# Kernel optimization log

Measured on AMD Instinct MI355X. Metric: run time of the kernel, lower is better.

## Reference

```python
import jax, jax.numpy as jnp
import numpy as np

B, N, D = 16, 2048, 64


def setup_inputs() -> dict:
    key = jax.random.key(0)
    kq, kk, kv = jax.random.split(key, 3)
    queries = jax.random.normal(kq, (B, N, D), dtype=jnp.float32)
    keys = jax.random.normal(kk, (B, N, D), dtype=jnp.float32)
    values = jax.random.normal(kv, (B, N, D), dtype=jnp.float32)
    return {"queries": queries, "keys": keys, "values": values}


def reference(queries, keys, values):
    d = queries.shape[-1]
    scale = 1.0 / jnp.sqrt(jnp.asarray(d, dtype=queries.dtype))
    # scores: [B, N, N] = Q @ K^T / sqrt(d)
    scores = jnp.einsum("bqd,bkd->bqk", queries, keys) * scale
    attn = jax.nn.softmax(scores, axis=-1)
    # dropout prob = 0.0 -> identity (inference-faithful)
    out = jnp.einsum("bqk,bkd->bqd", attn, values)
    return out
```

## Files before the change

kernel.cpp:

```cpp
#include <hip/hip_runtime.h>

typedef __attribute__((ext_vector_type(8)))  __bf16 bf16x8;
typedef __attribute__((ext_vector_type(4)))  __bf16 bf16x4;
typedef __attribute__((ext_vector_type(16))) float  f32x16;
typedef __attribute__((ext_vector_type(4)))  float  f32x4;

#define B_    16
#define N_    2048
#define D_    64
#define QBLK  128
#define KVBLK 64
#define NT    (N_ / KVBLK)
#define NG    4
#define TPG   (NT / NG)

#define VSTR    80
#define KSZ     8192
#define VASZ    5120
#define SLOT_SZ (KSZ + 2 * VASZ)
#define GRP_SZ  (2 * SLOT_SZ)
#define SMEM_SZ (NG * GRP_SZ)

static __device__ __forceinline__ float fast_exp2(float x) {
#if __has_builtin(__builtin_amdgcn_exp2f)
    return __builtin_amdgcn_exp2f(x);
#else
    return __expf(x * 0.6931471805599453f);
#endif
}

__global__ __attribute__((amdgpu_waves_per_eu(4, 4))) __launch_bounds__(1024)
void attn_fwd(const float* __restrict__ Qp, const float* __restrict__ Kp,
              const float* __restrict__ Vp, float* __restrict__ Op)
{
    __shared__ __align__(16) char smem[SMEM_SZ];

    const int tid  = threadIdx.x;
    const int wv   = tid >> 6;
    const int g    = tid >> 8;
    const int tg   = tid & 255;
    const int lane = tid & 63;
    const int w    = (tid >> 6) & 3;
    const int h    = lane >> 5;
    const int qcol = lane & 31;
    const int first  = (wv ^ (wv >> 2)) & 1;
    const int second = first ^ 1;

    const int bx    = blockIdx.x;
    const int batch = ((bx & 7) << 1) | ((bx >> 3) & 1);
    const int qtile = bx >> 4;
    const int q0w   = qtile * QBLK + w * 32;

    const float SL2E = 0.18033688011112042f;
    const size_t bboff = (size_t)batch * (N_ * D_);
    char* gbase = smem + g * GRP_SZ;

    const float* qrow = Qp + bboff + (size_t)(q0w + qcol) * D_ + h * 8;
    bf16x8 qf[4];
#pragma unroll
    for (int m = 0; m < 4; ++m) {
        f32x4 a = *reinterpret_cast<const f32x4*>(qrow + m * 16);
        f32x4 b = *reinterpret_cast<const f32x4*>(qrow + m * 16 + 4);
#pragma unroll
        for (int j = 0; j < 4; ++j) {
            qf[m][j]     = (__bf16)(a[j] * SL2E);
            qf[m][4 + j] = (__bf16)(b[j] * SL2E);
        }
    }

    const int krow = tg >> 3,  kcol = (tg & 7) * 8;
    const int vd   = tg & 63,  vkg  = tg >> 6;
    const int p1   = (vkg & 1) * 8 + (vkg >> 1) * 32;
    const int xorv = ((vd >> 3) & 3) << 4;
    const float* ksrc0 = Kp + bboff + (size_t)krow * D_ + kcol;
    const float* vsrc0 = Vp + bboff + (size_t)(vkg * 8) * D_ + vd;

    f32x4 kr[2];
    float vv[8];
    auto load_phase = [&](int t, int ph) {
        const float* ks = ksrc0 + ((size_t)t * KVBLK + ph * 32) * D_;
        const float* vs = vsrc0 + ((size_t)t * KVBLK + ph * 32) * D_;
        kr[0] = *reinterpret_cast<const f32x4*>(ks);
        kr[1] = *reinterpret_cast<const f32x4*>(ks + 4);
#pragma unroll
        for (int j = 0; j < 8; ++j) vv[j] = vs[(size_t)j * D_];
    };

    auto write_phase = [&](int b, int ph) {
        char* kb = gbase + b * SLOT_SZ;
        char* vb = kb + KSZ + ph * VASZ;
        bf16x8 w0;
#pragma unroll
        for (int j = 0; j < 4; ++j) { w0[j] = (__bf16)kr[0][j]; w0[4 + j] = (__bf16)kr[1][j]; }
        *reinterpret_cast<bf16x8*>(kb + (ph * 32 + krow) * 128 +
                                   ((kcol * 2) ^ ((krow & 7) << 4))) = w0;
        bf16x4 w1, w2;
#pragma unroll
        for (int j = 0; j < 4; ++j) { w1[j] = (__bf16)vv[j]; w2[j] = (__bf16)vv[4 + j]; }
        char* vrow = vb + vd * VSTR;
        *reinterpret_cast<bf16x4*>(vrow + ((p1)      ^ xorv)) = w1;
        *reinterpret_cast<bf16x4*>(vrow + ((p1 + 16) ^ xorv)) = w2;
    };

    f32x16 o0, o1;
#pragma unroll
    for (int i = 0; i < 16; ++i) { o0[i] = 0.f; o1[i] = 0.f; }
    float l_run = 0.f;

    const int kx  = (qcol & 7) << 4;
    const int vxr = ((qcol >> 3) & 3) << 4;

    auto do_sub = [&](const char* kb, int sub, int nxt, bool more) {
        f32x16 s;
#pragma unroll
        for (int i = 0; i < 16; ++i) s[i] = 0.f;
        __builtin_amdgcn_s_setprio(1);
#pragma unroll
        for (int m = 0; m < 4; ++m) {
            const int col = m * 32 + h * 16;
            bf16x8 k0 = *reinterpret_cast<const bf16x8*>(
                kb + (sub * 32 + qcol) * 128 + (col ^ kx));
            s = __builtin_amdgcn_mfma_f32_32x32x16_bf16(k0, qf[m], s, 0, 0, 0);
        }
        __builtin_amdgcn_s_setprio(0);

        float ps0 = 0.f, ps1 = 0.f, ps2 = 0.f, ps3 = 0.f;
        bf16x8 pfa, pfb;
#pragma unroll
        for (int i = 0; i < 4; ++i) {
            float p0 = fast_exp2(s[i]);
            float p1e = fast_exp2(s[4 + i]);
            float p2 = fast_exp2(s[8 + i]);
            float p3 = fast_exp2(s[12 + i]);
            ps0 += p0; ps1 += p1e; ps2 += p2; ps3 += p3;
            pfa[i] = (__bf16)p0; pfa[4 + i] = (__bf16)p1e;
            pfb[i] = (__bf16)p2; pfb[4 + i] = (__bf16)p3;
        }
        l_run += (ps0 + ps1) + (ps2 + ps3);

        if (more) write_phase(nxt, sub);

        const char* vb = kb + KSZ + sub * VASZ;
        __builtin_amdgcn_s_setprio(1);
#pragma unroll
        for (int db = 0; db < 2; ++db) {
            const char* vrowp = vb + (db * 32 + qcol) * VSTR;
            f32x16& oo = db ? o1 : o0;
#pragma unroll
            for (int sc = 0; sc < 2; ++sc) {
                bf16x8 vf = *reinterpret_cast<const bf16x8*>(
                    vrowp + ((h * 16 + sc * 32) ^ vxr));
                oo = __builtin_amdgcn_mfma_f32_32x32x16_bf16(vf, sc ? pfb : pfa, oo, 0, 0, 0);
            }
        }
        __builtin_amdgcn_s_setprio(0);
    };

    load_phase(g, 0);  write_phase(0, 0);
    load_phase(g, 1);  write_phase(0, 1);
    __syncthreads();

    for (int it = 0; it < TPG; ++it) {
        const int cur = it & 1;
        const int nxt = cur ^ 1;
        const bool more = (it + 1 < TPG);
        const int tn = NG * (it + 1) + g;
        const char* kb = gbase + cur * SLOT_SZ;

        if (more) load_phase(tn, first);
        do_sub(kb, first, nxt, more);
        if (more) load_phase(tn, second);
        do_sub(kb, second, nxt, more);
        __syncthreads();
    }

    float lt = l_run + __shfl_xor(l_run, 32);
    float* mlF  = (float*)smem;
    float* slab = (float*)smem;
    const int q  = w * 32 + qcol;

    if (h == 0) mlF[g * QBLK + q] = lt;
    __syncthreads();

    const float L = mlF[0 * QBLK + q] + mlF[1 * QBLK + q]
                  + mlF[2 * QBLK + q] + mlF[3 * QBLK + q];
    const float inv = 1.0f / L;
    __syncthreads();

    const int dl0 = 4 * h;
    auto slab_write = [&](float* sb, const f32x16& oo, int db) {
#pragma unroll
        for (int r = 0; r < 16; ++r) {
            const int d = db * 32 + (r & 3) + 8 * (r >> 2) + dl0;
            sb[d * 128 + q] = oo[r];
        }
    };
    auto slab_add = [&](const float* sb, f32x16& oo, int db) {
#pragma unroll
        for (int r = 0; r < 16; ++r) {
            const int d = db * 32 + (r & 3) + 8 * (r >> 2) + dl0;
            oo[r] += sb[d * 128 + q];
        }
    };

    if (g == 1) { slab_write(slab, o0, 0);        slab_write(slab, o1, 1); }
    if (g == 3) { slab_write(slab + 8192, o0, 0); slab_write(slab + 8192, o1, 1); }
    __syncthreads();

    if (g == 0) { slab_add(slab, o0, 0);        slab_add(slab, o1, 1); }
    if (g == 2) { slab_add(slab + 8192, o0, 0); slab_add(slab + 8192, o1, 1); }
    __syncthreads();

    if (g == 2) { slab_write(slab, o0, 0); slab_write(slab, o1, 1); }
    __syncthreads();

    if (g == 0) {
#pragma unroll
        for (int r = 0; r < 16; ++r) {
            const int d0 = (r & 3) + 8 * (r >> 2) + dl0;
            o0[r] = (o0[r] + slab[d0 * 128 + q]) * inv;
            o1[r] = (o1[r] + slab[(32 + d0) * 128 + q]) * inv;
        }
        float* orow = Op + bboff + (size_t)(q0w + qcol) * D_;
#pragma unroll
        for (int gg8 = 0; gg8 < 4; ++gg8) {
            f32x4 v, v2;
#pragma unroll
            for (int r = 0; r < 4; ++r) { v[r] = o0[4 * gg8 + r]; v2[r] = o1[4 * gg8 + r]; }
            *reinterpret_cast<f32x4*>(orow + gg8 * 8 + 4 * h)      = v;
            *reinterpret_cast<f32x4*>(orow + 32 + gg8 * 8 + 4 * h) = v2;
        }
    }
}

extern "C" void kernel_launch(void* const* d_in, const int* in_sizes, int n_in,
                              void* d_out, int out_size, void* d_ws, size_t ws_size,
                              hipStream_t stream) {
    const float* Q = (const float*)d_in[0];
    const float* K = (const float*)d_in[1];
    const float* V = (const float*)d_in[2];
    float* O = (float*)d_out;
    dim3 grid(256), block(1024);
    hipLaunchKernelGGL(attn_fwd, grid, block, 0, stream, Q, K, V, O);
}
```

Before: 34.02 us.

## Halve query and KV tiles, use 512-thread blocks with a single-subtile loop

```diff
diff --git a/kernel.cpp b/kernel.cpp
--- a/kernel.cpp
+++ b/kernel.cpp
@@ -8,16 +8,15 @@
 #define B_    16
 #define N_    2048
 #define D_    64
-#define QBLK  128
-#define KVBLK 64
+#define QBLK  64
+#define KVBLK 32
 #define NT    (N_ / KVBLK)
 #define NG    4
 #define TPG   (NT / NG)
 
 #define VSTR    80
-#define KSZ     8192
-#define VASZ    5120
-#define SLOT_SZ (KSZ + 2 * VASZ)
+#define KSZ     4096
+#define SLOT_SZ 9216
 #define GRP_SZ  (2 * SLOT_SZ)
 #define SMEM_SZ (NG * GRP_SZ)
 
@@ -29,7 +28,7 @@
 #endif
 }
 
-__global__ __attribute__((amdgpu_waves_per_eu(4, 4))) __launch_bounds__(1024)
+__global__ __attribute__((amdgpu_waves_per_eu(4, 4))) __launch_bounds__(512)
 void attn_fwd(const float* __restrict__ Qp, const float* __restrict__ Kp,
               const float* __restrict__ Vp, float* __restrict__ Op)
 {
@@ -37,14 +36,12 @@
 
     const int tid  = threadIdx.x;
     const int wv   = tid >> 6;
-    const int g    = tid >> 8;
-    const int tg   = tid & 255;
+    const int g    = wv >> 1;
+    const int w    = wv & 1;
+    const int tg   = tid & 127;
     const int lane = tid & 63;
-    const int w    = (tid >> 6) & 3;
     const int h    = lane >> 5;
     const int qcol = lane & 31;
-    const int first  = (wv ^ (wv >> 2)) & 1;
-    const int second = first ^ 1;
 
     const int bx    = blockIdx.x;
     const int batch = ((bx & 7) << 1) | ((bx >> 3) & 1);
@@ -69,17 +66,17 @@
     }
 
     const int krow = tg >> 3,  kcol = (tg & 7) * 8;
-    const int vd   = tg & 63,  vkg  = tg >> 6;
-    const int p1   = (vkg & 1) * 8 + (vkg >> 1) * 32;
+    const int vd   = tg & 63,  vkl  = tg >> 6;
+    const int p1l  = vkl * 8;
     const int xorv = ((vd >> 3) & 3) << 4;
     const float* ksrc0 = Kp + bboff + (size_t)krow * D_ + kcol;
-    const float* vsrc0 = Vp + bboff + (size_t)(vkg * 8) * D_ + vd;
+    const float* vsrc0 = Vp + bboff + (size_t)(vkl * 8) * D_ + vd;
 
     f32x4 kr[2];
     float vv[8];
     auto load_phase = [&](int t, int ph) {
-        const float* ks = ksrc0 + ((size_t)t * KVBLK + ph * 32) * D_;
-        const float* vs = vsrc0 + ((size_t)t * KVBLK + ph * 32) * D_;
+        const float* ks = ksrc0 + ((size_t)t * KVBLK + ph * 16) * D_;
+        const float* vs = vsrc0 + ((size_t)t * KVBLK + ph * 16) * D_;
         kr[0] = *reinterpret_cast<const f32x4*>(ks);
         kr[1] = *reinterpret_cast<const f32x4*>(ks + 4);
 #pragma unroll
@@ -88,16 +85,17 @@
 
     auto write_phase = [&](int b, int ph) {
         char* kb = gbase + b * SLOT_SZ;
-        char* vb = kb + KSZ + ph * VASZ;
+        char* vb = kb + KSZ;
         bf16x8 w0;
 #pragma unroll
         for (int j = 0; j < 4; ++j) { w0[j] = (__bf16)kr[0][j]; w0[4 + j] = (__bf16)kr[1][j]; }
-        *reinterpret_cast<bf16x8*>(kb + (ph * 32 + krow) * 128 +
+        *reinterpret_cast<bf16x8*>(kb + (ph * 16 + krow) * 128 +
                                    ((kcol * 2) ^ ((krow & 7) << 4))) = w0;
         bf16x4 w1, w2;
 #pragma unroll
         for (int j = 0; j < 4; ++j) { w1[j] = (__bf16)vv[j]; w2[j] = (__bf16)vv[4 + j]; }
         char* vrow = vb + vd * VSTR;
+        const int p1 = p1l + ph * 32;
         *reinterpret_cast<bf16x4*>(vrow + ((p1)      ^ xorv)) = w1;
         *reinterpret_cast<bf16x4*>(vrow + ((p1 + 16) ^ xorv)) = w2;
     };
@@ -110,7 +108,19 @@
     const int kx  = (qcol & 7) << 4;
     const int vxr = ((qcol >> 3) & 3) << 4;
 
-    auto do_sub = [&](const char* kb, int sub, int nxt, bool more) {
+    load_phase(g, 0);  write_phase(0, 0);
+    load_phase(g, 1);  write_phase(0, 1);
+    __syncthreads();
+
+    for (int it = 0; it < TPG; ++it) {
+        const int cur = it & 1;
+        const int nxt = cur ^ 1;
+        const bool more = (it + 1 < TPG);
+        const int tn = NG * (it + 1) + g;
+        const char* kb = gbase + cur * SLOT_SZ;
+
+        if (more) load_phase(tn, 0);
+
         f32x16 s;
 #pragma unroll
         for (int i = 0; i < 16; ++i) s[i] = 0.f;
@@ -118,8 +128,7 @@
 #pragma unroll
         for (int m = 0; m < 4; ++m) {
             const int col = m * 32 + h * 16;
-            bf16x8 k0 = *reinterpret_cast<const bf16x8*>(
-                kb + (sub * 32 + qcol) * 128 + (col ^ kx));
+            bf16x8 k0 = *reinterpret_cast<const bf16x8*>(kb + qcol * 128 + (col ^ kx));
             s = __builtin_amdgcn_mfma_f32_32x32x16_bf16(k0, qf[m], s, 0, 0, 0);
         }
         __builtin_amdgcn_s_setprio(0);
@@ -138,9 +147,9 @@
         }
         l_run += (ps0 + ps1) + (ps2 + ps3);
 
-        if (more) write_phase(nxt, sub);
-
-        const char* vb = kb + KSZ + sub * VASZ;
+        if (more) { write_phase(nxt, 0); load_phase(tn, 1); }
+
+        const char* vb = kb + KSZ;
         __builtin_amdgcn_s_setprio(1);
 #pragma unroll
         for (int db = 0; db < 2; ++db) {
@@ -154,23 +163,8 @@
             }
         }
         __builtin_amdgcn_s_setprio(0);
-    };
-
-    load_phase(g, 0);  write_phase(0, 0);
-    load_phase(g, 1);  write_phase(0, 1);
-    __syncthreads();
-
-    for (int it = 0; it < TPG; ++it) {
-        const int cur = it & 1;
-        const int nxt = cur ^ 1;
-        const bool more = (it + 1 < TPG);
-        const int tn = NG * (it + 1) + g;
-        const char* kb = gbase + cur * SLOT_SZ;
-
-        if (more) load_phase(tn, first);
-        do_sub(kb, first, nxt, more);
-        if (more) load_phase(tn, second);
-        do_sub(kb, second, nxt, more);
+
+        if (more) write_phase(nxt, 1);
         __syncthreads();
     }
 
@@ -192,23 +186,23 @@
 #pragma unroll
         for (int r = 0; r < 16; ++r) {
             const int d = db * 32 + (r & 3) + 8 * (r >> 2) + dl0;
-            sb[d * 128 + q] = oo[r];
+            sb[d * QBLK + q] = oo[r];
         }
     };
     auto slab_add = [&](const float* sb, f32x16& oo, int db) {
 #pragma unroll
         for (int r = 0; r < 16; ++r) {
             const int d = db * 32 + (r & 3) + 8 * (r >> 2) + dl0;
-            oo[r] += sb[d * 128 + q];
+            oo[r] += sb[d * QBLK + q];
         }
     };
 
     if (g == 1) { slab_write(slab, o0, 0);        slab_write(slab, o1, 1); }
-    if (g == 3) { slab_write(slab + 8192, o0, 0); slab_write(slab + 8192, o1, 1); }
+    if (g == 3) { slab_write(slab + 4096, o0, 0); slab_write(slab + 4096, o1, 1); }
     __syncthreads();
 
     if (g == 0) { slab_add(slab, o0, 0);        slab_add(slab, o1, 1); }
-    if (g == 2) { slab_add(slab + 8192, o0, 0); slab_add(slab + 8192, o1, 1); }
+    if (g == 2) { slab_add(slab + 4096, o0, 0); slab_add(slab + 4096, o1, 1); }
     __syncthreads();
 
     if (g == 2) { slab_write(slab, o0, 0); slab_write(slab, o1, 1); }
@@ -218,8 +212,8 @@
 #pragma unroll
         for (int r = 0; r < 16; ++r) {
             const int d0 = (r & 3) + 8 * (r >> 2) + dl0;
-            o0[r] = (o0[r] + slab[d0 * 128 + q]) * inv;
-            o1[r] = (o1[r] + slab[(32 + d0) * 128 + q]) * inv;
+            o0[r] = (o0[r] + slab[d0 * QBLK + q]) * inv;
+            o1[r] = (o1[r] + slab[(32 + d0) * QBLK + q]) * inv;
         }
         float* orow = Op + bboff + (size_t)(q0w + qcol) * D_;
 #pragma unroll
@@ -240,6 +234,6 @@
     const float* K = (const float*)d_in[1];
     const float* V = (const float*)d_in[2];
     float* O = (float*)d_out;
-    dim3 grid(256), block(1024);
+    dim3 grid(512), block(512);
     hipLaunchKernelGGL(attn_fwd, grid, block, 0, stream, Q, K, V, O);
 }
```

Measured after the change: 40.86 us. 20.1% more time.
